# Optimization experiments

Hardware: AMD Instinct MI355X
Metric: run time of the kernel (lower is better)

Reference implementation:

```python
import jax, jax.numpy as jnp
from jax import lax
import numpy as np

T, I, H, H2 = 2048, 64, 256, 1024  # time steps, input feats, hidden, hidden2


def _lstm(x, Wih, Whh, bih, bhh):
    """PyTorch-convention LSTM. x: [T, B, I]; Wih: [4H, I]; Whh: [4H, H].
    Gate order i, f, g, o. Returns hidden states [T, B, H]."""
    Hd = Whh.shape[1]
    b = bih + bhh
    xw = jnp.einsum('tbi,gi->tbg', x, Wih) + b  # precompute input projections

    def step(carry, xt):
        h, c = carry
        z = xt + h @ Whh.T
        i, f, g, o = jnp.split(z, 4, axis=-1)
        c = jax.nn.sigmoid(f) * c + jax.nn.sigmoid(i) * jnp.tanh(g)
        h = jax.nn.sigmoid(o) * jnp.tanh(c)
        return (h, c), h

    h0 = jnp.zeros((x.shape[1], Hd), x.dtype)
    _, hs = lax.scan(step, (h0, h0), xw)
    return hs


def setup_inputs() -> dict:
    key = jax.random.key(0)
    ks = jax.random.split(key, 16)
    s1 = 1.0 / np.sqrt(H)
    s2 = 1.0 / np.sqrt(H2)
    d = {
        'x': jax.random.normal(ks[0], (T, I, 21), jnp.float32),
        'Wih1': jax.random.uniform(ks[1], (4 * H, I), jnp.float32, -s1, s1),
        'Whh1': jax.random.uniform(ks[2], (4 * H, H), jnp.float32, -s1, s1),
        'bih1': jax.random.uniform(ks[3], (4 * H,), jnp.float32, -s1, s1),
        'bhh1': jax.random.uniform(ks[4], (4 * H,), jnp.float32, -s1, s1),
        'Wih2': jax.random.uniform(ks[5], (4 * H2, H * 21), jnp.float32, -s2, s2),
        'Whh2': jax.random.uniform(ks[6], (4 * H2, H2), jnp.float32, -s2, s2),
        'bih2': jax.random.uniform(ks[7], (4 * H2,), jnp.float32, -s2, s2),
        'bhh2': jax.random.uniform(ks[8], (4 * H2,), jnp.float32, -s2, s2),
        'Wih3': jax.random.uniform(ks[9], (4 * H, H2), jnp.float32, -s1, s1),
        'Whh3': jax.random.uniform(ks[10], (4 * H, H), jnp.float32, -s1, s1),
        'bih3': jax.random.uniform(ks[11], (4 * H,), jnp.float32, -s1, s1),
        'bhh3': jax.random.uniform(ks[12], (4 * H,), jnp.float32, -s1, s1),
        'Wfc': jax.random.uniform(ks[13], (21, H), jnp.float32, -s1, s1),
        'bfc': jax.random.uniform(ks[14], (21,), jnp.float32, -s1, s1),
    }
    return d


def reference(x, Wih1, Whh1, bih1, bhh1, Wih2, Whh2, bih2, bhh2,
              Wih3, Whh3, bih3, bhh3, Wfc, bfc):
    # The 21-iteration torch loop runs lstm1 independently on each of the 21
    # channel slices with batch=1; fold the 21 channels into the batch dim.
    x1 = jnp.transpose(x, (0, 2, 1))           # [T, 21, I]
    h1 = _lstm(x1, Wih1, Whh1, bih1, bhh1)     # [T, 21, H]
    # x_torch[:, :, i*H:(i+1)*H] = channel i -> channel-major concat
    xcat = h1.reshape(T, 1, 21 * H)            # [T, 1, 21H]
    h2 = _lstm(xcat, Wih2, Whh2, bih2, bhh2)   # [T, 1, H2]
    h3 = _lstm(h2, Wih3, Whh3, bih3, bhh3)     # [T, 1, H]
    out = h3 @ Wfc.T + bfc                     # [T, 1, 21]
    return out
```

## Files before the change

### kernel.cpp

```cpp
#include <hip/hip_runtime.h>


#define T_STEPS 2048
#define SENT 0xFFFFFFFFu

using f4v   = __attribute__((ext_vector_type(4))) float;
using s8v   = __attribute__((ext_vector_type(8))) short;
using u16x8 = __attribute__((ext_vector_type(8))) unsigned short;
using u32x4 = __attribute__((ext_vector_type(4))) unsigned;

__device__ __forceinline__ unsigned short f2bf(float v) {
  unsigned u = __float_as_uint(v);
  u = (u + 0x7FFFu + ((u >> 16) & 1u)) >> 16;
  return (unsigned short)u;
}
__device__ __forceinline__ float bf2f(unsigned short b) {
  return __uint_as_float(((unsigned)b) << 16);
}
__device__ __forceinline__ unsigned packhl(float v) {
  unsigned short hb = f2bf(v);
  unsigned short lb = f2bf(v - bf2f(hb));
  return (((unsigned)hb) << 16) | lb;
}
__device__ __forceinline__ float unpackhl(unsigned p) {
  return __uint_as_float(p & 0xFFFF0000u) + __uint_as_float(p << 16);
}
__device__ __forceinline__ float sigm(float x) { return 1.0f / (1.0f + __expf(-x)); }
__device__ __forceinline__ float tanh_f(float x) {
  float ax = fabsf(x);
  float e = __expf(-2.0f * ax);
  float t = (1.0f - e) / (1.0f + e);
  return copysignf(t, x);
}
__device__ __forceinline__ unsigned ld_agent32(const unsigned* p) {
  return __hip_atomic_load(p, __ATOMIC_RELAXED, __HIP_MEMORY_SCOPE_AGENT);
}
__device__ __forceinline__ void st_agent32(unsigned* p, unsigned v) {
  __hip_atomic_store(p, v, __ATOMIC_RELAXED, __HIP_MEMORY_SCOPE_AGENT);
}
__device__ __forceinline__ void ctr_add(unsigned* p) {
  __hip_atomic_fetch_add(p, 1u, __ATOMIC_RELAXED, __HIP_MEMORY_SCOPE_AGENT);
}
__device__ __forceinline__ void poll_ctr(const unsigned* p, unsigned tgt) {
  unsigned n = 0;
  while (ld_agent32(p) < tgt) {
    if (++n > (1u << 22)) break;
    __builtin_amdgcn_s_sleep(4);
  }
}
__device__ __forceinline__ u32x4 ld16_coh(const unsigned* addr) {
  u32x4 c;
  asm volatile("global_load_dwordx4 %0, %1, off sc0 sc1\n\t"
               "s_waitcnt vmcnt(0)"
               : "=&v"(c) : "v"(addr) : "memory");
  return c;
}
#define VMCNT0() asm volatile("s_waitcnt vmcnt(0)" ::: "memory")

#define ISSUE4(r0, r1, r2, r3, ad)                                          \
  asm volatile(                                                             \
      "global_load_dwordx4 %0, %4, off sc0 sc1\n\t"                         \
      "global_load_dwordx4 %1, %4, off offset:1024 sc0 sc1\n\t"             \
      "global_load_dwordx4 %2, %4, off offset:2048 sc0 sc1\n\t"             \
      "global_load_dwordx4 %3, %4, off offset:3072 sc0 sc1"                 \
      : "=&v"(r0), "=&v"(r1), "=&v"(r2), "=&v"(r3) : "v"(ad) : "memory")
#define OK4(r0, r1, r2, r3)                                                 \
  ((r0[0] != SENT) && (r0[1] != SENT) && (r0[2] != SENT) && (r0[3] != SENT) && \
   (r1[0] != SENT) && (r1[1] != SENT) && (r1[2] != SENT) && (r1[3] != SENT) && \
   (r2[0] != SENT) && (r2[1] != SENT) && (r2[2] != SENT) && (r2[3] != SENT) && \
   (r3[0] != SENT) && (r3[1] != SENT) && (r3[2] != SENT) && (r3[3] != SENT))

#define L16(M) M(0) M(1) M(2) M(3) M(4) M(5) M(6) M(7) M(8) M(9) M(10) M(11) \
  M(12) M(13) M(14) M(15)
#define L32(M) L16(M) M(16) M(17) M(18) M(19) M(20) M(21) M(22) M(23) M(24) \
  M(25) M(26) M(27) M(28) M(29) M(30) M(31)
#define L64(M) L32(M) M(32) M(33) M(34) M(35) M(36) \
  M(37) M(38) M(39) M(40) M(41) M(42) M(43) M(44) M(45) M(46) M(47) M(48) \
  M(49) M(50) M(51) M(52) M(53) M(54) M(55) M(56) M(57) M(58) M(59) M(60) \
  M(61) M(62) M(63)

__device__ __forceinline__ void unpack8(u32x4 a, u32x4 b, u16x8& hi, u16x8& lo) {
#pragma unroll
  for (int j = 0; j < 4; ++j) {
    hi[j]     = (unsigned short)(a[j] >> 16);
    lo[j]     = (unsigned short)(a[j] & 0xFFFFu);
    hi[4 + j] = (unsigned short)(b[j] >> 16);
    lo[4 + j] = (unsigned short)(b[j] & 0xFFFFu);
  }
}

__device__ void gemm_tile_packed(
    const unsigned* __restrict__ Ap, const unsigned short* __restrict__ Bh,
    const unsigned short* __restrict__ Bl, const float* __restrict__ b1,
    const float* __restrict__ b2, unsigned* __restrict__ C,
    int tm, int tn, int K, int N, char* smem)
{
  unsigned short* lds = (unsigned short*)smem;
  const size_t m0 = (size_t)tm * 128, n0 = (size_t)tn * 128;
  const int tid = threadIdx.x, lane = tid & 63, w = tid >> 6;
  const int wr = w >> 1, wc = w & 1;
  const int srow = tid >> 2, sc8 = (tid & 3) * 8;

  const unsigned* pA = Ap + m0 * K;
  const unsigned short* pBh = Bh + n0 * K;
  const unsigned short* pBl = Bl + n0 * K;

  f4v acc[4][4];
#pragma unroll
  for (int i = 0; i < 4; ++i)
#pragma unroll
    for (int j = 0; j < 4; ++j) acc[i][j] = f4v{0.f, 0.f, 0.f, 0.f};

  u32x4 a00, a01, a10, a11;
  u16x8 s4, s5, s6, s7;
#define LOADK(k0)                                                                    \
  a00 = __builtin_nontemporal_load((const u32x4*)(pA + (size_t)srow * K + (k0) + sc8));        \
  a01 = __builtin_nontemporal_load((const u32x4*)(pA + (size_t)srow * K + (k0) + sc8 + 4));    \
  a10 = __builtin_nontemporal_load((const u32x4*)(pA + (size_t)(srow + 64) * K + (k0) + sc8)); \
  a11 = __builtin_nontemporal_load((const u32x4*)(pA + (size_t)(srow + 64) * K + (k0) + sc8 + 4)); \
  s4 = __builtin_nontemporal_load((const u16x8*)(pBh + (size_t)srow * K + (k0) + sc8));        \
  s5 = __builtin_nontemporal_load((const u16x8*)(pBh + (size_t)(srow + 64) * K + (k0) + sc8)); \
  s6 = __builtin_nontemporal_load((const u16x8*)(pBl + (size_t)srow * K + (k0) + sc8));        \
  s7 = __builtin_nontemporal_load((const u16x8*)(pBl + (size_t)(srow + 64) * K + (k0) + sc8));

  LOADK(0);
  const int fr = lane & 15, fko = (lane >> 4) * 8;
  for (int k0 = 0; k0 < K; k0 += 32) {
    u16x8 h0, l0, h1, l1;
    unpack8(a00, a01, h0, l0);
    unpack8(a10, a11, h1, l1);
    *(u16x8*)&lds[0     +  srow       * 32 + sc8] = h0;
    *(u16x8*)&lds[0     + (srow + 64) * 32 + sc8] = h1;
    *(u16x8*)&lds[4096  +  srow       * 32 + sc8] = l0;
    *(u16x8*)&lds[4096  + (srow + 64) * 32 + sc8] = l1;
    *(u16x8*)&lds[8192  +  srow       * 32 + sc8] = s4;
    *(u16x8*)&lds[8192  + (srow + 64) * 32 + sc8] = s5;
    *(u16x8*)&lds[12288 +  srow       * 32 + sc8] = s6;
    *(u16x8*)&lds[12288 + (srow + 64) * 32 + sc8] = s7;
    __syncthreads();
    if (k0 + 32 < K) { LOADK(k0 + 32); }
    s8v afh[4], afl[4], bfh[4], bfl[4];
#pragma unroll
    for (int i = 0; i < 4; ++i) {
      int ar = (64 * wr + 16 * i + fr) * 32 + fko;
      int br = (64 * wc + 16 * i + fr) * 32 + fko;
      afh[i] = *(const s8v*)&lds[0 + ar];
      afl[i] = *(const s8v*)&lds[4096 + ar];
      bfh[i] = *(const s8v*)&lds[8192 + br];
      bfl[i] = *(const s8v*)&lds[12288 + br];
    }
#pragma unroll
    for (int mi = 0; mi < 4; ++mi)
#pragma unroll
      for (int ni = 0; ni < 4; ++ni) {
        acc[mi][ni] = __builtin_amdgcn_mfma_f32_16x16x32_bf16(afh[mi], bfh[ni], acc[mi][ni], 0, 0, 0);
        acc[mi][ni] = __builtin_amdgcn_mfma_f32_16x16x32_bf16(afh[mi], bfl[ni], acc[mi][ni], 0, 0, 0);
        acc[mi][ni] = __builtin_amdgcn_mfma_f32_16x16x32_bf16(afl[mi], bfh[ni], acc[mi][ni], 0, 0, 0);
      }
    __syncthreads();
  }
#undef LOADK
  const int er = (lane >> 4) * 4, ec = lane & 15;
#pragma unroll
  for (int ni = 0; ni < 4; ++ni) {
    size_t col = n0 + 64 * wc + 16 * ni + ec;
    float bv = b1[col] + b2[col];
#pragma unroll
    for (int mi = 0; mi < 4; ++mi) {
      size_t row = m0 + 64 * wr + 16 * mi + er;
#pragma unroll
      for (int rr = 0; rr < 4; ++rr)
        st_agent32(&C[(row + rr) * N + col], __float_as_uint(acc[mi][ni][rr] + bv));
    }
  }
}

__global__ __launch_bounds__(256, 1) void mega_kernel(
    const float* __restrict__ x,
    const float* __restrict__ Wih1, const float* __restrict__ Whh1,
    const float* __restrict__ bih1, const float* __restrict__ bhh1,
    const float* __restrict__ Whh2,
    const float* __restrict__ bih2, const float* __restrict__ bhh2,
    const float* __restrict__ Whh3,
    const float* __restrict__ bih3, const float* __restrict__ bhh3,
    unsigned* __restrict__ h1r0, unsigned* __restrict__ h2r0,
    unsigned* __restrict__ h3r0, unsigned* __restrict__ cnt,
    unsigned* __restrict__ h1rows, unsigned* __restrict__ h2rows,
    unsigned* __restrict__ h3rows,
    float* __restrict__ xw2, float* __restrict__ xw3,
    const unsigned short* __restrict__ wih2h, const unsigned short* __restrict__ wih2l,
    const unsigned short* __restrict__ wih3h, const unsigned short* __restrict__ wih3l)
{
  __shared__ __align__(16) char smem[32768];
  unsigned* ready1 = cnt + 0;
  unsigned* done2  = cnt + 16;
  unsigned* ready2 = cnt + 32;
  unsigned* done3  = cnt + 48;
  const int wg = blockIdx.x;
  const int widx = threadIdx.x >> 6, lane = threadIdx.x & 63;

  if (wg < 84) {
    const int c = wg / 4, sub = wg % 4;
    const int gwv = sub * 4 + widx;
    const int u16i = lane & 15, g = lane >> 4;
    const int grow = g * 256 + gwv * 16 + u16i;

    const f4v* wsrc = (const f4v*)(Whh1 + (size_t)grow * 256);
    const f4v* xsrc = (const f4v*)(Wih1 + (size_t)grow * 64);
#define DH(i) f4v m##i = wsrc[i];
#define DX(i) f4v n##i = xsrc[i];
    L64(DH)
    L16(DX)
#undef DH
#undef DX
    const float bias = bih1[grow] + bhh1[grow];

    float* const hb = (float*)smem + widx * 320;
    float* const xq = hb + 256;

    float cst = 0.0f;
    float xpre = x[(size_t)lane * 21 + c];

    for (int t = 0; t < T_STEPS; ++t) {
      xq[lane] = xpre;
      if (t + 1 < T_STEPS) xpre = x[(size_t)(t + 1) * 1344 + lane * 21 + c];
      const unsigned* src = t ? h1rows + (size_t)(t - 1) * 5376 + c * 256
                              : h1r0 + c * 256;
      const unsigned* addr = src + 4 * lane;
      u32x4 c0;
      unsigned n = 0;
      for (;;) {
        c0 = ld16_coh(addr);
        bool ok = (c0[0] != SENT) && (c0[1] != SENT) &&
                  (c0[2] != SENT) && (c0[3] != SENT);
        if (ok || ++n > (1u << 18)) break;
      }
      *(f4v*)&hb[4 * lane] = f4v{unpackhl(c0[0]), unpackhl(c0[1]),
                                 unpackhl(c0[2]), unpackhl(c0[3])};
      float a0 = 0, a1 = 0, a2 = 0, a3 = 0;
#define FH(i) { f4v h4 = *(const f4v*)&hb[4 * i]; \
  a0 = fmaf(m##i[0], h4[0], a0); a1 = fmaf(m##i[1], h4[1], a1); \
  a2 = fmaf(m##i[2], h4[2], a2); a3 = fmaf(m##i[3], h4[3], a3); }
#define FX(i) { f4v x4 = *(const f4v*)&xq[4 * i]; \
  a0 = fmaf(n##i[0], x4[0], a0); a1 = fmaf(n##i[1], x4[1], a1); \
  a2 = fmaf(n##i[2], x4[2], a2); a3 = fmaf(n##i[3], x4[3], a3); }
      L64(FH)
      L16(FX)
#undef FH
#undef FX
      float z = (a0 + a1) + (a2 + a3) + bias;
      float zi = __shfl(z, u16i);
      float zf = __shfl(z, 16 + u16i);
      float zg = __shfl(z, 32 + u16i);
      float zo = __shfl(z, 48 + u16i);
      if (lane < 16) {
        float cn = sigm(zf) * cst + sigm(zi) * tanh_f(zg);
        float hn = sigm(zo) * tanh_f(cn);
        cst = cn;
        st_agent32(&h1rows[(size_t)t * 5376 + c * 256 + gwv * 16 + lane], packhl(hn));
      }
      if ((t & 127) == 127) {
        VMCNT0();
        if (lane == 0) ctr_add(&ready1[t >> 7]);
      }
    }
  } else if (wg < 212) {
    const int gw = (wg - 84) * 4 + widx;
    const int r8 = lane >> 3, e = lane & 7;
    const int g = r8 >> 1, u = r8 & 1;
    const int grow = g * 1024 + 2 * gw + u;

    const f4v* wsrc = (const f4v*)(Whh2 + (size_t)grow * 1024 + e * 128);
#define DW(i) f4v w##i = wsrc[i];
    L32(DW)
#undef DW
    asm volatile("" : "+v"(w0), "+v"(w1), "+v"(w2), "+v"(w3),
                      "+v"(w4), "+v"(w5), "+v"(w6), "+v"(w7));
    asm volatile("" : "+v"(w8), "+v"(w9), "+v"(w10), "+v"(w11),
                      "+v"(w12), "+v"(w13), "+v"(w14), "+v"(w15));
    asm volatile("" : "+v"(w16), "+v"(w17), "+v"(w18), "+v"(w19),
                      "+v"(w20), "+v"(w21), "+v"(w22), "+v"(w23));
    asm volatile("" : "+v"(w24), "+v"(w25), "+v"(w26), "+v"(w27),
                      "+v"(w28), "+v"(w29), "+v"(w30), "+v"(w31));

    float* const hls = (float*)smem + widx * 1060;
    const float* const eb = hls + e * 132;
    const int sb = (lane >> 5) * 132 + 4 * (lane & 31);
    const int ug = lane & 1;

    float cst = 0.0f;
    float xwi = 0, xwf = 0, xwg = 0, xwo = 0;
    if (lane < 2) {
      xwi = xw2[0 * 4096 + 0 * 1024 + 2 * gw + lane];
    }

    for (int t = 0; t < T_STEPS; ++t) {
      if ((t & 127) == 0) {
        poll_ctr(&done2[t >> 7], 32);
        if (lane < 2) {
          const float* xp = xw2 + (size_t)t * 4096 + 2 * gw + lane;
          xwi = xp[0]; xwf = xp[1024]; xwg = xp[2048]; xwo = xp[3072];
        }
      }
      {
        const unsigned* src = t ? h2rows + (size_t)(t - 1) * 1024 : h2r0;
        const unsigned* addr = src + 4 * lane;
        u32x4 c0, c1, c2, c3;
        unsigned n = 0;
        for (;;) {
          ISSUE4(c0, c1, c2, c3, addr);
          asm volatile("s_waitcnt vmcnt(0)"
                       : "+v"(c0), "+v"(c1), "+v"(c2), "+v"(c3) :: "memory");
          if (OK4(c0, c1, c2, c3) || ++n > (1u << 18)) break;
        }
        *(f4v*)&hls[sb]       = f4v{unpackhl(c0[0]), unpackhl(c0[1]), unpackhl(c0[2]), unpackhl(c0[3])};
        *(f4v*)&hls[sb + 264] = f4v{unpackhl(c1[0]), unpackhl(c1[1]), unpackhl(c1[2]), unpackhl(c1[3])};
        *(f4v*)&hls[sb + 528] = f4v{unpackhl(c2[0]), unpackhl(c2[1]), unpackhl(c2[2]), unpackhl(c2[3])};
        *(f4v*)&hls[sb + 792] = f4v{unpackhl(c3[0]), unpackhl(c3[1]), unpackhl(c3[2]), unpackhl(c3[3])};
      }
      float a0 = 0, a1 = 0, a2 = 0, a3 = 0;
#define FW(i) { f4v h4 = *(const f4v*)&eb[4 * i]; \
  a0 = fmaf(w##i[0], h4[0], a0); a1 = fmaf(w##i[1], h4[1], a1); \
  a2 = fmaf(w##i[2], h4[2], a2); a3 = fmaf(w##i[3], h4[3], a3); }
      L32(FW)
#undef FW
      float z = (a0 + a1) + (a2 + a3);
      z += __shfl_xor(z, 1);
      z += __shfl_xor(z, 2);
      z += __shfl_xor(z, 4);
      float zi = __shfl(z, (0 + ug) * 8);
      float zf = __shfl(z, (2 + ug) * 8);
      float zg2 = __shfl(z, (4 + ug) * 8);
      float zo = __shfl(z, (6 + ug) * 8);
      if (lane < 2) {
        float vi = zi + xwi, vf = zf + xwf, vg = zg2 + xwg, vo = zo + xwo;
        float cn = sigm(vf) * cst + sigm(vi) * tanh_f(vg);
        float hn = sigm(vo) * tanh_f(cn);
        cst = cn;
        st_agent32(&h2rows[(size_t)t * 1024 + 2 * gw + lane], packhl(hn));
      }
      if ((t & 127) == 127) {
        VMCNT0();
        if (lane == 0) ctr_add(&ready2[t >> 7]);
      }
      if (lane < 2 && t + 1 < T_STEPS && ((t + 1) & 127) != 0) {
        const float* xp = xw2 + (size_t)(t + 1) * 4096 + 2 * gw + lane;
        xwi = xp[0]; xwf = xp[1024]; xwg = xp[2048]; xwo = xp[3072];
      }
    }
  } else if (wg < 216) {
    const int gw = (wg - 212) * 4 + widx;
    const int u16i = lane & 15, g = lane >> 4;
    const int grow = g * 256 + gw * 16 + u16i;

    const f4v* wsrc = (const f4v*)(Whh3 + (size_t)grow * 256);
#define DW(i) f4v w##i = wsrc[i];
    L64(DW)
#undef DW

    float* const hb = (float*)smem + widx * 256;
    float cst = 0.0f;
    float xwn = 0.0f;

    for (int t = 0; t < T_STEPS; ++t) {
      float xwv;
      if ((t & 127) == 0) {
        poll_ctr(&done3[t >> 7], 8);
        xwv = xw3[(size_t)t * 1024 + grow];
      } else xwv = xwn;
      const unsigned* src = t ? h3rows + (size_t)(t - 1) * 256 : h3r0;
      const unsigned* addr = src + 4 * lane;
      u32x4 c0;
      unsigned n = 0;
      for (;;) {
        c0 = ld16_coh(addr);
        bool ok = (c0[0] != SENT) && (c0[1] != SENT) &&
                  (c0[2] != SENT) && (c0[3] != SENT);
        if (ok || ++n > (1u << 18)) break;
      }
      *(f4v*)&hb[4 * lane] = f4v{__uint_as_float(c0[0]), __uint_as_float(c0[1]),
                                 __uint_as_float(c0[2]), __uint_as_float(c0[3])};
      float a0 = 0, a1 = 0, a2 = 0, a3 = 0;
#define FW(i) { f4v h4 = *(const f4v*)&hb[4 * i]; \
  a0 = fmaf(w##i[0], h4[0], a0); a1 = fmaf(w##i[1], h4[1], a1); \
  a2 = fmaf(w##i[2], h4[2], a2); a3 = fmaf(w##i[3], h4[3], a3); }
      L64(FW)
#undef FW
      float z = (a0 + a1) + (a2 + a3) + xwv;
      float zi = __shfl(z, u16i);
      float zf = __shfl(z, 16 + u16i);
      float zg = __shfl(z, 32 + u16i);
      float zo = __shfl(z, 48 + u16i);
      if (lane < 16) {
        float cn = sigm(zf) * cst + sigm(zi) * tanh_f(zg);
        float hn = sigm(zo) * tanh_f(cn);
        cst = cn;
        st_agent32(&h3rows[(size_t)t * 256 + gw * 16 + lane], __float_as_uint(hn));
      }
      if (t + 1 < T_STEPS && ((t + 1) & 127) != 0)
        xwn = xw3[(size_t)(t + 1) * 1024 + grow];
    }
  } else if (wg < 244) {
    const int pw = wg - 216;
    for (int i = pw; i < 512; i += 28) {
      int tm = i >> 5, tn = i & 31;
      poll_ctr(&ready1[tm], 336);
      gemm_tile_packed(h1rows, wih2h, wih2l, bih2, bhh2,
                       (unsigned*)xw2, tm, tn, 5376, 4096, smem);
      VMCNT0();
      __syncthreads();
      if (threadIdx.x == 0) ctr_add(&done2[tm]);
      __syncthreads();
    }
  } else {
    const int pw = wg - 244;
    for (int i = pw; i < 128; i += 8) {
      int tm = i >> 3, tn = i & 7;
      poll_ctr(&ready2[tm], 512);
      gemm_tile_packed(h2rows, wih3h, wih3l, bih3, bhh3,
                       (unsigned*)xw3, tm, tn, 1024, 1024, smem);
      VMCNT0();
      __syncthreads();
      if (threadIdx.x == 0) ctr_add(&done3[tm]);
      __syncthreads();
    }
  }
}

__global__ void split_kernel(const float* __restrict__ src,
                             unsigned short* __restrict__ hi,
                             unsigned short* __restrict__ lo, int n) {
  int i = blockIdx.x * 256 + threadIdx.x;
  if (i < n) {
    float v = src[i];
    unsigned short hb = f2bf(v);
    hi[i] = hb;
    lo[i] = f2bf(v - bf2f(hb));
  }
}

__global__ void fc_kernel(const float* __restrict__ h3, const float* __restrict__ Wfc,
                          const float* __restrict__ bfc, float* __restrict__ out) {
  int t = blockIdx.x, m = threadIdx.x;
  if (m < 21) {
    const float* hp = h3 + (size_t)t * 256;
    const float* wp = Wfc + m * 256;
    float a = 0.0f;
#pragma unroll 8
    for (int j = 0; j < 256; ++j) a = fmaf(wp[j], hp[j], a);
    out[t * 21 + m] = a + bfc[m];
  }
}

extern "C" void kernel_launch(void* const* d_in, const int* in_sizes, int n_in,
                              void* d_out, int out_size, void* d_ws, size_t ws_size,
                              hipStream_t stream) {
  const float* x    = (const float*)d_in[0];
  const float* Wih1 = (const float*)d_in[1];
  const float* Whh1 = (const float*)d_in[2];
  const float* bih1 = (const float*)d_in[3];
  const float* bhh1 = (const float*)d_in[4];
  const float* Wih2 = (const float*)d_in[5];
  const float* Whh2 = (const float*)d_in[6];
  const float* bih2 = (const float*)d_in[7];
  const float* bhh2 = (const float*)d_in[8];
  const float* Wih3 = (const float*)d_in[9];
  const float* Whh3 = (const float*)d_in[10];
  const float* bih3 = (const float*)d_in[11];
  const float* bhh3 = (const float*)d_in[12];
  const float* Wfc  = (const float*)d_in[13];
  const float* bfc  = (const float*)d_in[14];
  float* out = (float*)d_out;

  const size_t WS_NEEDED = 188776448;
  if (ws_size < WS_NEEDED) return;
  char* ws = (char*)d_ws;
  unsigned* h1r0 = (unsigned*)(ws + 0);
  unsigned* h2r0 = (unsigned*)(ws + 21504);
  unsigned* h3r0 = (unsigned*)(ws + 25600);
  unsigned* cnt  = (unsigned*)(ws + 26624);
  unsigned* h1rows = (unsigned*)(ws + 32768);
  unsigned* h2rows = (unsigned*)(ws + 44072960);
  unsigned* h3rows = (unsigned*)(ws + 52461568);
  float* xw2 = (float*)(ws + 54558720);
  float* xw3 = (float*)(ws + 88113152);
  unsigned short* wih2h = (unsigned short*)(ws + 96501760);
  unsigned short* wih2l = (unsigned short*)(ws + 140541952);
  unsigned short* wih3h = (unsigned short*)(ws + 184582144);
  unsigned short* wih3l = (unsigned short*)(ws + 186679296);

  hipMemsetAsync(ws, 0, 32768, stream);
  hipMemsetAsync(ws + 32768, 0xFF, 54525952, stream);

  const int nW2 = 4096 * 5376;
  split_kernel<<<(nW2 + 255) / 256, 256, 0, stream>>>(Wih2, wih2h, wih2l, nW2);
  const int nW3 = 1024 * 1024;
  split_kernel<<<(nW3 + 255) / 256, 256, 0, stream>>>(Wih3, wih3h, wih3l, nW3);

  mega_kernel<<<252, 256, 0, stream>>>(
      x, Wih1, Whh1, bih1, bhh1,
      Whh2, bih2, bhh2, Whh3, bih3, bhh3,
      h1r0, h2r0, h3r0, cnt,
      h1rows, h2rows, h3rows, xw2, xw3,
      wih2h, wih2l, wih3h, wih3l);

  fc_kernel<<<2048, 64, 0, stream>>>((const float*)h3rows, Wfc, bfc, out);
}
```

Measured before the change: 10.71 ms.

## Halve pipeline chunk to 64 timesteps and raise priority on recurrent critical path

Shrinks the producer/consumer chunk between the recurrent layers and the in-kernel projection GEMMs from 128 to 64 timesteps. To match, it uses a 64-row GEMM tile, doubles the tile count and counter spacing, and shrinks LDS. It also wraps the recurrent compute in s_setprio so the latency-critical recurrence waves get issue priority over co-resident GEMM work. The aim is less pipeline fill/drain latency between stages, at the cost of more synchronisation events and smaller, less efficient GEMM tiles. It also drops nontemporal hints on GEMM loads.

After: 9.943 ms, median of 3. -7.1%, faster.

```diff
diff --git a/kernel.cpp b/kernel.cpp
--- a/kernel.cpp
+++ b/kernel.cpp
@@ -89,14 +89,14 @@
   }
 }
 
-__device__ void gemm_tile_packed(
+__device__ void gemm_tile_packed64(
     const unsigned* __restrict__ Ap, const unsigned short* __restrict__ Bh,
     const unsigned short* __restrict__ Bl, const float* __restrict__ b1,
     const float* __restrict__ b2, unsigned* __restrict__ C,
     int tm, int tn, int K, int N, char* smem)
 {
   unsigned short* lds = (unsigned short*)smem;
-  const size_t m0 = (size_t)tm * 128, n0 = (size_t)tn * 128;
+  const size_t m0 = (size_t)tm * 64, n0 = (size_t)tn * 128;
   const int tid = threadIdx.x, lane = tid & 63, w = tid >> 6;
   const int wr = w >> 1, wc = w & 1;
   const int srow = tid >> 2, sc8 = (tid & 3) * 8;
@@ -105,52 +105,50 @@
   const unsigned short* pBh = Bh + n0 * K;
   const unsigned short* pBl = Bl + n0 * K;
 
-  f4v acc[4][4];
-#pragma unroll
-  for (int i = 0; i < 4; ++i)
+  f4v acc[2][4];
+#pragma unroll
+  for (int i = 0; i < 2; ++i)
 #pragma unroll
     for (int j = 0; j < 4; ++j) acc[i][j] = f4v{0.f, 0.f, 0.f, 0.f};
 
-  u32x4 a00, a01, a10, a11;
+  u32x4 a00, a01;
   u16x8 s4, s5, s6, s7;
-#define LOADK(k0)                                                                    \
-  a00 = __builtin_nontemporal_load((const u32x4*)(pA + (size_t)srow * K + (k0) + sc8));        \
-  a01 = __builtin_nontemporal_load((const u32x4*)(pA + (size_t)srow * K + (k0) + sc8 + 4));    \
-  a10 = __builtin_nontemporal_load((const u32x4*)(pA + (size_t)(srow + 64) * K + (k0) + sc8)); \
-  a11 = __builtin_nontemporal_load((const u32x4*)(pA + (size_t)(srow + 64) * K + (k0) + sc8 + 4)); \
-  s4 = __builtin_nontemporal_load((const u16x8*)(pBh + (size_t)srow * K + (k0) + sc8));        \
-  s5 = __builtin_nontemporal_load((const u16x8*)(pBh + (size_t)(srow + 64) * K + (k0) + sc8)); \
-  s6 = __builtin_nontemporal_load((const u16x8*)(pBl + (size_t)srow * K + (k0) + sc8));        \
-  s7 = __builtin_nontemporal_load((const u16x8*)(pBl + (size_t)(srow + 64) * K + (k0) + sc8));
+#define LOADK(k0)                                                           \
+  a00 = *(const u32x4*)(pA + (size_t)srow * K + (k0) + sc8);                \
+  a01 = *(const u32x4*)(pA + (size_t)srow * K + (k0) + sc8 + 4);            \
+  s4 = *(const u16x8*)(pBh + (size_t)srow * K + (k0) + sc8);                \
+  s5 = *(const u16x8*)(pBh + (size_t)(srow + 64) * K + (k0) + sc8);         \
+  s6 = *(const u16x8*)(pBl + (size_t)srow * K + (k0) + sc8);                \
+  s7 = *(const u16x8*)(pBl + (size_t)(srow + 64) * K + (k0) + sc8);
 
   LOADK(0);
   const int fr = lane & 15, fko = (lane >> 4) * 8;
   for (int k0 = 0; k0 < K; k0 += 32) {
-    u16x8 h0, l0, h1, l1;
+    u16x8 h0, l0;
     unpack8(a00, a01, h0, l0);
-    unpack8(a10, a11, h1, l1);
-    *(u16x8*)&lds[0     +  srow       * 32 + sc8] = h0;
-    *(u16x8*)&lds[0     + (srow + 64) * 32 + sc8] = h1;
-    *(u16x8*)&lds[4096  +  srow       * 32 + sc8] = l0;
-    *(u16x8*)&lds[4096  + (srow + 64) * 32 + sc8] = l1;
-    *(u16x8*)&lds[8192  +  srow       * 32 + sc8] = s4;
-    *(u16x8*)&lds[8192  + (srow + 64) * 32 + sc8] = s5;
-    *(u16x8*)&lds[12288 +  srow       * 32 + sc8] = s6;
-    *(u16x8*)&lds[12288 + (srow + 64) * 32 + sc8] = s7;
+    *(u16x8*)&lds[0     + srow * 32 + sc8] = h0;
+    *(u16x8*)&lds[2048  + srow * 32 + sc8] = l0;
+    *(u16x8*)&lds[4096  +  srow       * 32 + sc8] = s4;
+    *(u16x8*)&lds[4096  + (srow + 64) * 32 + sc8] = s5;
+    *(u16x8*)&lds[8192  +  srow       * 32 + sc8] = s6;
+    *(u16x8*)&lds[8192  + (srow + 64) * 32 + sc8] = s7;
     __syncthreads();
     if (k0 + 32 < K) { LOADK(k0 + 32); }
-    s8v afh[4], afl[4], bfh[4], bfl[4];
+    s8v afh[2], afl[2], bfh[4], bfl[4];
+#pragma unroll
+    for (int i = 0; i < 2; ++i) {
+      int ar = (32 * wr + 16 * i + fr) * 32 + fko;
+      afh[i] = *(const s8v*)&lds[0 + ar];
+      afl[i] = *(const s8v*)&lds[2048 + ar];
+    }
 #pragma unroll
     for (int i = 0; i < 4; ++i) {
-      int ar = (64 * wr + 16 * i + fr) * 32 + fko;
       int br = (64 * wc + 16 * i + fr) * 32 + fko;
-      afh[i] = *(const s8v*)&lds[0 + ar];
-      afl[i] = *(const s8v*)&lds[4096 + ar];
-      bfh[i] = *(const s8v*)&lds[8192 + br];
-      bfl[i] = *(const s8v*)&lds[12288 + br];
-    }
-#pragma unroll
-    for (int mi = 0; mi < 4; ++mi)
+      bfh[i] = *(const s8v*)&lds[4096 + br];
+      bfl[i] = *(const s8v*)&lds[8192 + br];
+    }
+#pragma unroll
+    for (int mi = 0; mi < 2; ++mi)
 #pragma unroll
       for (int ni = 0; ni < 4; ++ni) {
         acc[mi][ni] = __builtin_amdgcn_mfma_f32_16x16x32_bf16(afh[mi], bfh[ni], acc[mi][ni], 0, 0, 0);
@@ -166,8 +164,8 @@
     size_t col = n0 + 64 * wc + 16 * ni + ec;
     float bv = b1[col] + b2[col];
 #pragma unroll
-    for (int mi = 0; mi < 4; ++mi) {
-      size_t row = m0 + 64 * wr + 16 * mi + er;
+    for (int mi = 0; mi < 2; ++mi) {
+      size_t row = m0 + 32 * wr + 16 * mi + er;
 #pragma unroll
       for (int rr = 0; rr < 4; ++rr)
         st_agent32(&C[(row + rr) * N + col], __float_as_uint(acc[mi][ni][rr] + bv));
@@ -191,11 +189,11 @@
     const unsigned short* __restrict__ wih2h, const unsigned short* __restrict__ wih2l,
     const unsigned short* __restrict__ wih3h, const unsigned short* __restrict__ wih3l)
 {
-  __shared__ __align__(16) char smem[32768];
+  __shared__ __align__(16) char smem[24576];
   unsigned* ready1 = cnt + 0;
-  unsigned* done2  = cnt + 16;
-  unsigned* ready2 = cnt + 32;
-  unsigned* done3  = cnt + 48;
+  unsigned* done2  = cnt + 32;
+  unsigned* ready2 = cnt + 64;
+  unsigned* done3  = cnt + 96;
   const int wg = blockIdx.x;
   const int widx = threadIdx.x >> 6, lane = threadIdx.x & 63;
 
@@ -235,6 +233,7 @@
                   (c0[2] != SENT) && (c0[3] != SENT);
         if (ok || ++n > (1u << 18)) break;
       }
+      __builtin_amdgcn_s_setprio(1);
       *(f4v*)&hb[4 * lane] = f4v{unpackhl(c0[0]), unpackhl(c0[1]),
                                  unpackhl(c0[2]), unpackhl(c0[3])};
       float a0 = 0, a1 = 0, a2 = 0, a3 = 0;
@@ -259,9 +258,10 @@
         cst = cn;
         st_agent32(&h1rows[(size_t)t * 5376 + c * 256 + gwv * 16 + lane], packhl(hn));
       }
-      if ((t & 127) == 127) {
+      __builtin_amdgcn_s_setprio(0);
+      if ((t & 63) == 63) {
         VMCNT0();
-        if (lane == 0) ctr_add(&ready1[t >> 7]);
+        if (lane == 0) ctr_add(&ready1[t >> 6]);
       }
     }
   } else if (wg < 212) {
@@ -290,13 +290,10 @@
 
     float cst = 0.0f;
     float xwi = 0, xwf = 0, xwg = 0, xwo = 0;
-    if (lane < 2) {
-      xwi = xw2[0 * 4096 + 0 * 1024 + 2 * gw + lane];
-    }
 
     for (int t = 0; t < T_STEPS; ++t) {
-      if ((t & 127) == 0) {
-        poll_ctr(&done2[t >> 7], 32);
+      if ((t & 63) == 0) {
+        poll_ctr(&done2[t >> 6], 32);
         if (lane < 2) {
           const float* xp = xw2 + (size_t)t * 4096 + 2 * gw + lane;
           xwi = xp[0]; xwf = xp[1024]; xwg = xp[2048]; xwo = xp[3072];
@@ -313,6 +310,7 @@
                        : "+v"(c0), "+v"(c1), "+v"(c2), "+v"(c3) :: "memory");
           if (OK4(c0, c1, c2, c3) || ++n > (1u << 18)) break;
         }
+        __builtin_amdgcn_s_setprio(1);
         *(f4v*)&hls[sb]       = f4v{unpackhl(c0[0]), unpackhl(c0[1]), unpackhl(c0[2]), unpackhl(c0[3])};
         *(f4v*)&hls[sb + 264] = f4v{unpackhl(c1[0]), unpackhl(c1[1]), unpackhl(c1[2]), unpackhl(c1[3])};
         *(f4v*)&hls[sb + 528] = f4v{unpackhl(c2[0]), unpackhl(c2[1]), unpackhl(c2[2]), unpackhl(c2[3])};
@@ -339,11 +337,12 @@
         cst = cn;
         st_agent32(&h2rows[(size_t)t * 1024 + 2 * gw + lane], packhl(hn));
       }
-      if ((t & 127) == 127) {
+      __builtin_amdgcn_s_setprio(0);
+      if ((t & 63) == 63) {
         VMCNT0();
-        if (lane == 0) ctr_add(&ready2[t >> 7]);
-      }
-      if (lane < 2 && t + 1 < T_STEPS && ((t + 1) & 127) != 0) {
+        if (lane == 0) ctr_add(&ready2[t >> 6]);
+      }
+      if (lane < 2 && t + 1 < T_STEPS && ((t + 1) & 63) != 0) {
         const float* xp = xw2 + (size_t)(t + 1) * 4096 + 2 * gw + lane;
         xwi = xp[0]; xwf = xp[1024]; xwg = xp[2048]; xwo = xp[3072];
       }
@@ -364,8 +363,8 @@
 
     for (int t = 0; t < T_STEPS; ++t) {
       float xwv;
-      if ((t & 127) == 0) {
-        poll_ctr(&done3[t >> 7], 8);
+      if ((t & 63) == 0) {
+        poll_ctr(&done3[t >> 6], 8);
         xwv = xw3[(size_t)t * 1024 + grow];
       } else xwv = xwn;
       const unsigned* src = t ? h3rows + (size_t)(t - 1) * 256 : h3r0;
@@ -378,6 +377,7 @@
                   (c0[2] != SENT) && (c0[3] != SENT);
         if (ok || ++n > (1u << 18)) break;
       }
+      __builtin_amdgcn_s_setprio(1);
       *(f4v*)&hb[4 * lane] = f4v{__uint_as_float(c0[0]), __uint_as_float(c0[1]),
                                  __uint_as_float(c0[2]), __uint_as_float(c0[3])};
       float a0 = 0, a1 = 0, a2 = 0, a3 = 0;
@@ -397,16 +397,17 @@
         cst = cn;
         st_agent32(&h3rows[(size_t)t * 256 + gw * 16 + lane], __float_as_uint(hn));
       }
-      if (t + 1 < T_STEPS && ((t + 1) & 127) != 0)
+      __builtin_amdgcn_s_setprio(0);
+      if (t + 1 < T_STEPS && ((t + 1) & 63) != 0)
         xwn = xw3[(size_t)(t + 1) * 1024 + grow];
     }
   } else if (wg < 244) {
     const int pw = wg - 216;
-    for (int i = pw; i < 512; i += 28) {
+    for (int i = pw; i < 1024; i += 28) {
       int tm = i >> 5, tn = i & 31;
       poll_ctr(&ready1[tm], 336);
-      gemm_tile_packed(h1rows, wih2h, wih2l, bih2, bhh2,
-                       (unsigned*)xw2, tm, tn, 5376, 4096, smem);
+      gemm_tile_packed64(h1rows, wih2h, wih2l, bih2, bhh2,
+                         (unsigned*)xw2, tm, tn, 5376, 4096, smem);
       VMCNT0();
       __syncthreads();
       if (threadIdx.x == 0) ctr_add(&done2[tm]);
@@ -414,11 +415,11 @@
     }
   } else {
     const int pw = wg - 244;
-    for (int i = pw; i < 128; i += 8) {
+    for (int i = pw; i < 256; i += 8) {
       int tm = i >> 3, tn = i & 7;
       poll_ctr(&ready2[tm], 512);
-      gemm_tile_packed(h2rows, wih3h, wih3l, bih3, bhh3,
-                       (unsigned*)xw3, tm, tn, 1024, 1024, smem);
+      gemm_tile_packed64(h2rows, wih3h, wih3l, bih3, bhh3,
+                         (unsigned*)xw3, tm, tn, 1024, 1024, smem);
       VMCNT0();
       __syncthreads();
       if (threadIdx.x == 0) ctr_add(&done3[tm]);
```
